# Kernel tuning notes

Hardware: AMD Instinct MI355X
Metric: run time of the kernel (lower is better)

## Reference

```python
import jax, jax.numpy as jnp
import numpy as np

B, S, H = 2, 2048, 3072
NH, NKV, HD = 32, 8, 96
ROPE_THETA = 10000.0
NEG = -1e9


def setup_inputs() -> dict:
    key = jax.random.key(0)
    k0, k1, k2 = jax.random.split(key, 3)
    hidden_states = jax.random.normal(k0, (B, S, H), jnp.float32) * 0.02
    # rotary embeddings (precomputed, as HF passes position_embeddings=(cos,sin))
    inv_freq = 1.0 / (ROPE_THETA ** (jnp.arange(0, HD, 2, dtype=jnp.float32) / HD))
    pos = jnp.arange(S, dtype=jnp.float32)
    freqs = pos[:, None] * inv_freq[None, :]            # [S, HD/2]
    emb = jnp.concatenate([freqs, freqs], axis=-1)      # [S, HD]
    cos = jnp.broadcast_to(jnp.cos(emb)[None], (B, S, HD))
    sin = jnp.broadcast_to(jnp.sin(emb)[None], (B, S, HD))
    # additive causal mask [B,1,S,S]
    causal = jnp.tril(jnp.ones((S, S), dtype=bool))
    attention_mask = jnp.where(causal, 0.0, NEG).astype(jnp.float32)
    attention_mask = jnp.broadcast_to(attention_mask[None, None], (B, 1, S, S))
    Wqkv = jax.random.normal(k1, ((NH + 2 * NKV) * HD, H), jnp.float32) * 0.02
    Wo = jax.random.normal(k2, (H, NH * HD), jnp.float32) * 0.02
    cache_position = jnp.arange(S, dtype=jnp.int32)
    position_ids = jnp.broadcast_to(jnp.arange(S, dtype=jnp.int32)[None], (B, S))
    return {"hidden_states": hidden_states, "cos": cos, "sin": sin,
            "attention_mask": attention_mask, "Wqkv": Wqkv, "Wo": Wo,
            "cache_position": cache_position, "position_ids": position_ids}


def _rotate_half(x):
    x1, x2 = x[..., : HD // 2], x[..., HD // 2:]
    return jnp.concatenate([-x2, x1], axis=-1)


def reference(hidden_states, cos, sin, attention_mask, Wqkv, Wo, cache_position, position_ids):
    # fused qkv projection (no bias in Phi3)
    qkv = jnp.einsum('bsh,dh->bsd', hidden_states, Wqkv)  # [B,S,(NH+2*NKV)*HD]
    q = qkv[..., : NH * HD].reshape(B, S, NH, HD).transpose(0, 2, 1, 3)           # [B,NH,S,HD]
    k = qkv[..., NH * HD: (NH + NKV) * HD].reshape(B, S, NKV, HD).transpose(0, 2, 1, 3)
    v = qkv[..., (NH + NKV) * HD:].reshape(B, S, NKV, HD).transpose(0, 2, 1, 3)   # [B,NKV,S,HD]
    # rotary embedding (unsqueeze head dim)
    cosb, sinb = cos[:, None], sin[:, None]              # [B,1,S,HD]
    q = q * cosb + _rotate_half(q) * sinb
    k = k * cosb + _rotate_half(k) * sinb
    # DynamicCache() is empty -> cache update is identity (k, v unchanged)
    # GQA: repeat kv heads
    rep = NH // NKV
    k = jnp.repeat(k, rep, axis=1)                       # [B,NH,S,HD]
    v = jnp.repeat(v, rep, axis=1)
    # SDPA
    scale = 1.0 / jnp.sqrt(jnp.float32(HD))
    scores = jnp.einsum('bhqd,bhkd->bhqk', q, k) * scale + attention_mask
    attn = jax.nn.softmax(scores, axis=-1)
    ctx = jnp.einsum('bhqk,bhkd->bhqd', attn, v)         # [B,NH,S,HD]
    ctx = ctx.transpose(0, 2, 1, 3).reshape(B, S, NH * HD)
    out = jnp.einsum('bsd,hd->bsh', ctx, Wo)             # o_proj
    return out
```

## Files before the change

### kernel.cpp

```cpp
#include <hip/hip_runtime.h>

typedef __attribute__((ext_vector_type(8))) __bf16 bf16x8;
typedef __attribute__((ext_vector_type(4))) float f32x4;
typedef __attribute__((ext_vector_type(4))) unsigned int u32x4;
typedef __attribute__((ext_vector_type(4))) unsigned short u16x4;
typedef __attribute__((ext_vector_type(8))) unsigned short u16x8;

__device__ __forceinline__ unsigned short f2bf(float x) {
  unsigned u = __builtin_bit_cast(unsigned, x);
  u += 0x7fffu + ((u >> 16) & 1u);
  return (unsigned short)(u >> 16);
}
__device__ __forceinline__ float bf2f(unsigned short h) {
  unsigned u = ((unsigned)h) << 16;
  return __builtin_bit_cast(float, u);
}
__device__ __forceinline__ bf16x8 ld_frag(const unsigned short* p) {
  u32x4 u = *(const u32x4*)p;
  return __builtin_bit_cast(bf16x8, u);
}
__device__ __forceinline__ void gload_lds16(const unsigned short* g, unsigned short* l) {
  __builtin_amdgcn_global_load_lds(
      (const __attribute__((address_space(1))) void*)g,
      (__attribute__((address_space(3))) void*)l, 16, 0, 0);
}

__global__ __launch_bounds__(256) void cvt_bf16(const float* __restrict__ in,
                                                unsigned short* __restrict__ out, int n4) {
  int i = blockIdx.x * 256 + threadIdx.x;
  if (i >= n4) return;
  f32x4 v = *((const f32x4*)in + i);
  u16x4 o;
  #pragma unroll
  for (int j = 0; j < 4; ++j) o[j] = f2bf(v[j]);
  *((u16x4*)out + i) = o;
}

template <int MODE>
__global__ __launch_bounds__(512, 2) void gemm8p(const unsigned short* __restrict__ A,
                                                 const unsigned short* __restrict__ B,
                                                 void* __restrict__ Cv,
                                                 const float* __restrict__ cs,
                                                 const float* __restrict__ sn,
                                                 int M, int N, int K) {
  __shared__ __align__(16) unsigned short SM[57344];
  const int nwg = gridDim.x;
  const int swz = (blockIdx.x & 7) * (nwg >> 3) + (blockIdx.x >> 3);
  const int bx = swz & 15, by = swz >> 4;
  const int row0 = bx * 256, col0 = by * 192;
  const int tid = threadIdx.x;
  const int wave = tid >> 6, lane = tid & 63;
  const int g = lane >> 4, r = lane & 15;
  const int wm = (wave >> 1) * 64, wn = (wave & 1) * 96;
  const int NT = K >> 6;

  const unsigned short* Agb = A + (size_t)row0 * K;
  const unsigned short* Bgb = B + (size_t)col0 * K;

  f32x4 acc[4][6] = {};

  auto SU = [&](const unsigned short* src, unsigned short* dst, int u) {
    const int pos = u * 512 + tid;
    const int rw = pos >> 3, cc = pos & 7;
    gload_lds16(src + (size_t)rw * K + ((cc ^ (rw & 7)) * 8), dst + pos * 8);
  };
  auto LDA = [&](const unsigned short* base, int mi, int dk) {
    const int rw = wm + mi * 16 + r;
    return ld_frag(base + rw * 64 + (((dk * 4 + g) ^ (r & 7)) * 8));
  };
  auto LDB = [&](const unsigned short* base, int ni, int dk) {
    const int rw = wn + ni * 16 + r;
    return ld_frag(base + rw * 64 + (((dk * 4 + g) ^ (r & 7)) * 8));
  };

  SU(Agb, SM, 0); SU(Agb, SM, 1); SU(Agb, SM, 2); SU(Agb, SM, 3);
  SU(Bgb, SM + 16384, 0); SU(Bgb, SM + 16384, 1); SU(Bgb, SM + 16384, 2);
  __syncthreads();

  for (int t = 0; t < NT; ++t) {
    const int d = t & 1;
    const unsigned short* Ab = SM + d * 28672;
    const unsigned short* Bb = Ab + 16384;
    unsigned short* An = SM + (d ^ 1) * 28672;
    unsigned short* Bn = An + 16384;
    const unsigned short* Asrc = Agb + (t + 1) * 64;
    const unsigned short* Bsrc = Bgb + (t + 1) * 64;
    const bool pf = (t + 1 < NT);

    bf16x8 a0, a1, b[6];

    b[0] = LDB(Bb, 0, 0); b[1] = LDB(Bb, 1, 0); b[2] = LDB(Bb, 2, 0);
    b[3] = LDB(Bb, 3, 0); b[4] = LDB(Bb, 4, 0); b[5] = LDB(Bb, 5, 0);
    a0 = LDA(Ab, 0, 0); a1 = LDA(Ab, 1, 0);
    if (pf) { SU(Asrc, An, 0); SU(Asrc, An, 1); SU(Asrc, An, 2); }
    __builtin_amdgcn_s_barrier();
    asm volatile("s_waitcnt lgkmcnt(0)" ::: "memory");
    __builtin_amdgcn_sched_barrier(0);
    __builtin_amdgcn_s_setprio(1);
    #pragma unroll
    for (int n = 0; n < 6; ++n) {
      acc[0][n] = __builtin_amdgcn_mfma_f32_16x16x32_bf16(a0, b[n], acc[0][n], 0, 0, 0);
      acc[1][n] = __builtin_amdgcn_mfma_f32_16x16x32_bf16(a1, b[n], acc[1][n], 0, 0, 0);
    }
    __builtin_amdgcn_s_setprio(0);
    __builtin_amdgcn_s_barrier();

    a0 = LDA(Ab, 2, 0); a1 = LDA(Ab, 3, 0);
    if (pf) { SU(Asrc, An, 3); SU(Bsrc, Bn, 0); }
    __builtin_amdgcn_s_barrier();
    asm volatile("s_waitcnt lgkmcnt(0)" ::: "memory");
    __builtin_amdgcn_sched_barrier(0);
    __builtin_amdgcn_s_setprio(1);
    #pragma unroll
    for (int n = 0; n < 6; ++n) {
      acc[2][n] = __builtin_amdgcn_mfma_f32_16x16x32_bf16(a0, b[n], acc[2][n], 0, 0, 0);
      acc[3][n] = __builtin_amdgcn_mfma_f32_16x16x32_bf16(a1, b[n], acc[3][n], 0, 0, 0);
    }
    __builtin_amdgcn_s_setprio(0);
    __builtin_amdgcn_s_barrier();

    b[0] = LDB(Bb, 0, 1); b[1] = LDB(Bb, 1, 1); b[2] = LDB(Bb, 2, 1);
    b[3] = LDB(Bb, 3, 1); b[4] = LDB(Bb, 4, 1); b[5] = LDB(Bb, 5, 1);
    a0 = LDA(Ab, 0, 1); a1 = LDA(Ab, 1, 1);
    if (pf) { SU(Bsrc, Bn, 1); SU(Bsrc, Bn, 2); }
    __builtin_amdgcn_s_barrier();
    asm volatile("s_waitcnt lgkmcnt(0)" ::: "memory");
    __builtin_amdgcn_sched_barrier(0);
    __builtin_amdgcn_s_setprio(1);
    #pragma unroll
    for (int n = 0; n < 6; ++n) {
      acc[0][n] = __builtin_amdgcn_mfma_f32_16x16x32_bf16(a0, b[n], acc[0][n], 0, 0, 0);
      acc[1][n] = __builtin_amdgcn_mfma_f32_16x16x32_bf16(a1, b[n], acc[1][n], 0, 0, 0);
    }
    __builtin_amdgcn_s_setprio(0);
    __builtin_amdgcn_s_barrier();

    a0 = LDA(Ab, 2, 1); a1 = LDA(Ab, 3, 1);
    __builtin_amdgcn_s_barrier();
    asm volatile("s_waitcnt lgkmcnt(0)" ::: "memory");
    __builtin_amdgcn_sched_barrier(0);
    __builtin_amdgcn_s_setprio(1);
    #pragma unroll
    for (int n = 0; n < 6; ++n) {
      acc[2][n] = __builtin_amdgcn_mfma_f32_16x16x32_bf16(a0, b[n], acc[2][n], 0, 0, 0);
      acc[3][n] = __builtin_amdgcn_mfma_f32_16x16x32_bf16(a1, b[n], acc[3][n], 0, 0, 0);
    }
    __builtin_amdgcn_s_setprio(0);
    asm volatile("s_waitcnt vmcnt(0)" ::: "memory");
    __builtin_amdgcn_s_barrier();
  }

  if (MODE == 0) {
    float* outp = (float*)Cv;
    #pragma unroll
    for (int mi = 0; mi < 4; ++mi)
      #pragma unroll
      for (int n = 0; n < 6; ++n)
        #pragma unroll
        for (int rr = 0; rr < 4; ++rr) {
          const size_t idx = (size_t)(row0 + wm + mi * 16 + g * 4 + rr) * (size_t)N
                           + (col0 + wn + n * 16 + r);
          outp[idx] = acc[mi][n][rr];
        }
  } else {
    unsigned short* outp = (unsigned short*)Cv;
    const int hc0 = col0 + wn;
    if (hc0 < 3840) {
      #pragma unroll
      for (int mi = 0; mi < 4; ++mi)
        #pragma unroll
        for (int rr = 0; rr < 4; ++rr) {
          const int row = row0 + wm + mi * 16 + g * 4 + rr;
          const int cb = row * 96;
          const size_t rb = (size_t)row * N + hc0;
          #pragma unroll
          for (int n = 0; n < 3; ++n) {
            const int d = n * 16 + r;
            const float x1 = acc[mi][n][rr], x2 = acc[mi][n + 3][rr];
            const float c1 = cs[cb + d], s1 = sn[cb + d];
            const float c2 = cs[cb + d + 48], s2 = sn[cb + d + 48];
            outp[rb + d]      = f2bf(x1 * c1 - x2 * s1);
            outp[rb + d + 48] = f2bf(x2 * c2 + x1 * s2);
          }
        }
    } else {
      #pragma unroll
      for (int mi = 0; mi < 4; ++mi)
        #pragma unroll
        for (int n = 0; n < 6; ++n)
          #pragma unroll
          for (int rr = 0; rr < 4; ++rr) {
            const size_t idx = (size_t)(row0 + wm + mi * 16 + g * 4 + rr) * (size_t)N
                             + (col0 + wn + n * 16 + r);
            outp[idx] = f2bf(acc[mi][n][rr]);
          }
    }
  }
}

__global__ __launch_bounds__(256) void vtrans(const unsigned short* __restrict__ qkv,
                                              unsigned short* __restrict__ vt) {
  __shared__ __align__(16) unsigned short T[64 * 104];
  const int s0 = blockIdx.x * 64;
  const int kvh = blockIdx.y, b = blockIdx.z;
  const int tid = threadIdx.x;
  #pragma unroll
  for (int it = 0; it < 3; ++it) {
    const int c = it * 256 + tid;
    const int sr = c / 12, d0 = (c % 12) * 8;
    *(u32x4*)&T[sr * 104 + d0] =
        *(const u32x4*)&qkv[(size_t)(b * 2048 + s0 + sr) * 4608 + 3840 + kvh * 96 + d0];
  }
  __syncthreads();
  #pragma unroll
  for (int it = 0; it < 3; ++it) {
    const int c = it * 256 + tid;
    const int dr = c >> 3, k0 = (c & 7) * 8;
    u16x8 o;
    #pragma unroll
    for (int j = 0; j < 8; ++j) o[j] = T[(k0 + j) * 104 + dr];
    *(u16x8*)&vt[((size_t)(b * 8 + kvh) * 96 + dr) * 2048 + s0 + k0] = o;
  }
}

__global__ __launch_bounds__(512) void attn_fwd(const unsigned short* __restrict__ qkv,
                                                const unsigned short* __restrict__ vt,
                                                unsigned short* __restrict__ ctx) {
  __shared__ __align__(16) unsigned short SMEM[40960];
  const int wg = blockIdx.x;
  const int xcd = wg & 7, j = wg >> 3;
  const int c = xcd + ((j >> 4) << 3);
  const int b = c >> 3, kvh = c & 7;
  const int rj = j & 15;
  const int h = kvh * 4 + (rj >> 2);
  const int pr = rj & 3;
  const int tid = threadIdx.x;
  const int wave = tid >> 6, lane = tid & 63;
  const int g = lane >> 4, r = lane & 15;
  const float kLS = 0.14724445f;

  const unsigned short* kgbase = qkv + (size_t)(b * 2048) * 4608 + 3072 + kvh * 96;
  const unsigned short* vgbase = vt + (size_t)(b * 8 + kvh) * 96 * 2048;

  auto STAGE = [&](int t, int bi) {
    const int kv0 = t * 64;
    unsigned short* kd = SMEM + bi * 6144;
    unsigned short* vd = SMEM + 12288 + bi * 6144;
    #pragma unroll
    for (int i = 0; i < 3; ++i) {
      const int l = i * 512 + tid;
      if (l < 768) {
        const int dk = l >> 8, rem = l & 255;
        const int row = rem >> 2, cc = rem & 3;
        const int csrc = cc ^ ((row >> 1) & 3);
        gload_lds16(kgbase + (size_t)(kv0 + row) * 4608 + dk * 32 + csrc * 8, kd + l * 8);
      } else {
        const int lv = l - 768;
        const int row = lv >> 3, cc = lv & 7;
        const int csrc = cc ^ (row & 7);
        gload_lds16(vgbase + (size_t)row * 2048 + kv0 + csrc * 8, vd + lv * 8);
      }
    }
  };

  #pragma unroll 1
  for (int sel = 0; sel < 2; ++sel) {
    const int qt = sel ? pr : 7 - pr;
    const int nt = qt * 4 + 4;
    const int q0 = qt * 256 + wave * 32;

    __syncthreads();

    bf16x8 qf[2][3];
    #pragma unroll
    for (int qb = 0; qb < 2; ++qb)
      #pragma unroll
      for (int dk = 0; dk < 3; ++dk)
        qf[qb][dk] = ld_frag(&qkv[(size_t)(b * 2048 + q0 + qb * 16 + r) * 4608 + h * 96 + dk * 32 + g * 8]);

    f32x4 o[6][2] = {};
    float m_[2] = {-1e30f, -1e30f};
    float l_[2] = {0.f, 0.f};

    STAGE(0, 0);
    __syncthreads();

    for (int t = 0; t < nt; ++t) {
      const int cur = t & 1;
      if (t + 1 < nt) STAGE(t + 1, cur ^ 1);
      const int kv0 = t * 64;
      const unsigned short* Ks = SMEM + cur * 6144;
      const unsigned short* Vs = SMEM + 12288 + cur * 6144;
      unsigned short* Ps = SMEM + 24576 + wave * 2048;

      if (kv0 <= q0 + 31) {
        f32x4 st[4][2] = {};
        #pragma unroll
        for (int dk = 0; dk < 3; ++dk) {
          bf16x8 af[4];
          #pragma unroll
          for (int kb = 0; kb < 4; ++kb)
            af[kb] = ld_frag(&Ks[dk * 2048 + (kb * 16 + r) * 32 + ((g ^ ((r >> 1) & 3)) * 8)]);
          __builtin_amdgcn_s_setprio(1);
          #pragma unroll
          for (int kb = 0; kb < 4; ++kb)
            #pragma unroll
            for (int qb = 0; qb < 2; ++qb)
              st[kb][qb] = __builtin_amdgcn_mfma_f32_16x16x32_bf16(af[kb], qf[qb][dk], st[kb][qb], 0, 0, 0);
          __builtin_amdgcn_s_setprio(0);
        }
        if (kv0 + 63 > q0) {
          #pragma unroll
          for (int kb = 0; kb < 4; ++kb)
            #pragma unroll
            for (int qb = 0; qb < 2; ++qb)
              #pragma unroll
              for (int rr = 0; rr < 4; ++rr) {
                const int ka = kv0 + kb * 16 + g * 4 + rr;
                const int qa = q0 + qb * 16 + r;
                const float s = st[kb][qb][rr] * kLS;
                st[kb][qb][rr] = (ka <= qa) ? s : -1e30f;
              }
        } else {
          #pragma unroll
          for (int kb = 0; kb < 4; ++kb)
            #pragma unroll
            for (int qb = 0; qb < 2; ++qb)
              #pragma unroll
              for (int rr = 0; rr < 4; ++rr)
                st[kb][qb][rr] *= kLS;
        }
        #pragma unroll
        for (int qb = 0; qb < 2; ++qb) {
          float mx = st[0][qb][0];
          #pragma unroll
          for (int kb = 0; kb < 4; ++kb)
            #pragma unroll
            for (int rr = 0; rr < 4; ++rr) mx = fmaxf(mx, st[kb][qb][rr]);
          mx = fmaxf(mx, __shfl_xor(mx, 16));
          mx = fmaxf(mx, __shfl_xor(mx, 32));
          if (__all(mx <= m_[qb])) {
            float rs = 0.f;
            #pragma unroll
            for (int kb = 0; kb < 4; ++kb)
              #pragma unroll
              for (int rr = 0; rr < 4; ++rr) {
                const float p = __builtin_amdgcn_exp2f(st[kb][qb][rr] - m_[qb]);
                st[kb][qb][rr] = p;
                rs += p;
              }
            rs += __shfl_xor(rs, 16);
            rs += __shfl_xor(rs, 32);
            l_[qb] += rs;
          } else {
            const float mnew = fmaxf(m_[qb], mx);
            const float corr = __builtin_amdgcn_exp2f(m_[qb] - mnew);
            m_[qb] = mnew;
            float rs = 0.f;
            #pragma unroll
            for (int kb = 0; kb < 4; ++kb)
              #pragma unroll
              for (int rr = 0; rr < 4; ++rr) {
                const float p = __builtin_amdgcn_exp2f(st[kb][qb][rr] - mnew);
                st[kb][qb][rr] = p;
                rs += p;
              }
            rs += __shfl_xor(rs, 16);
            rs += __shfl_xor(rs, 32);
            l_[qb] = l_[qb] * corr + rs;
            #pragma unroll
            for (int db = 0; db < 6; ++db) o[db][qb] *= corr;
          }
        }
        #pragma unroll
        for (int kb = 0; kb < 4; ++kb)
          #pragma unroll
          for (int qb = 0; qb < 2; ++qb) {
            u16x4 w;
            #pragma unroll
            for (int rr = 0; rr < 4; ++rr) w[rr] = f2bf(st[kb][qb][rr]);
            const int q = qb * 16 + r;
            *(u16x4*)&Ps[q * 64 + (((2 * kb + (g >> 1)) ^ (r & 7)) << 3) + (g & 1) * 4] = w;
          }
        #pragma unroll
        for (int kk = 0; kk < 2; ++kk) {
          bf16x8 pb[2];
          #pragma unroll
          for (int qb = 0; qb < 2; ++qb)
            pb[qb] = ld_frag(&Ps[(qb * 16 + r) * 64 + ((kk * 4 + g) ^ (r & 7)) * 8]);
          __builtin_amdgcn_s_setprio(1);
          #pragma unroll
          for (int db = 0; db < 6; ++db) {
            const bf16x8 va = ld_frag(&Vs[(db * 16 + r) * 64 + ((kk * 4 + g) ^ (r & 7)) * 8]);
            #pragma unroll
            for (int qb = 0; qb < 2; ++qb)
              o[db][qb] = __builtin_amdgcn_mfma_f32_16x16x32_bf16(va, pb[qb], o[db][qb], 0, 0, 0);
          }
          __builtin_amdgcn_s_setprio(0);
        }
      }
      __syncthreads();
    }

    const float inv_l[2] = {1.f / l_[0], 1.f / l_[1]};
    unsigned short* obuf = SMEM + wave * 3328;
    #pragma unroll
    for (int db = 0; db < 6; ++db)
      #pragma unroll
      for (int qb = 0; qb < 2; ++qb) {
        u16x4 w;
        #pragma unroll
        for (int rr = 0; rr < 4; ++rr) w[rr] = f2bf(o[db][qb][rr] * inv_l[qb]);
        *(u16x4*)&obuf[(qb * 16 + r) * 104 + db * 16 + g * 4] = w;
      }
    #pragma unroll
    for (int it = 0; it < 6; ++it) {
      const int cc = it * 64 + lane;
      const int qr = cc / 12, d0 = (cc % 12) * 8;
      *(u32x4*)&ctx[(size_t)(b * 2048 + q0 + qr) * 3072 + h * 96 + d0] =
          *(const u32x4*)&obuf[qr * 104 + d0];
    }
  }
}

extern "C" void kernel_launch(void* const* d_in, const int* in_sizes, int n_in,
                              void* d_out, int out_size, void* d_ws, size_t ws_size,
                              hipStream_t stream) {
  const float* hs   = (const float*)d_in[0];
  const float* cosp = (const float*)d_in[1];
  const float* sinp = (const float*)d_in[2];
  const float* wqkv = (const float*)d_in[4];
  const float* wo   = (const float*)d_in[5];
  float* out = (float*)d_out;

  unsigned short* qkv = (unsigned short*)d_ws;
  unsigned short* hsb = qkv + 18874368;
  unsigned short* wqb = hsb + 12582912;
  unsigned short* vt  = hsb;
  unsigned short* wob = hsb + 3145728;
  unsigned short* ctx = wqb;

  cvt_bf16<<<12288, 256, 0, stream>>>(hs,   hsb, 3145728);
  cvt_bf16<<<13824, 256, 0, stream>>>(wqkv, wqb, 3538944);
  gemm8p<1><<<384, 512, 0, stream>>>(hsb, wqb, (void*)qkv, cosp, sinp, 4096, 4608, 3072);
  vtrans<<<dim3(32, 8, 2), 256, 0, stream>>>(qkv, vt);
  cvt_bf16<<<9216, 256, 0, stream>>>(wo, wob, 2359296);
  attn_fwd<<<256, 512, 0, stream>>>(qkv, vt, ctx);
  gemm8p<0><<<256, 512, 0, stream>>>(ctx, wob, (void*)out, cosp, sinp, 4096, 3072, 3072);
}
```

Baseline: 342.3 us.

## Add 4-wave 128x192-tile GEMM for QKV projection with RoPE epilogue

Adds a new gemm4w kernel using 256-thread blocks with a 128x192 output tile and a double-buffered LDS pipeline, and uses it for the fused QKV projection plus RoPE instead of the 8-wave gemm8p. The grid doubles to 768 smaller workgroups, which improves wave-quantization and load balance across CUs and may allow more blocks per CU. In exchange each block reuses less data, so global/LDS traffic per FLOP rises.

Result: slower. 402.6 us (+17.6%).

```diff
diff --git a/kernel.cpp b/kernel.cpp
--- a/kernel.cpp
+++ b/kernel.cpp
@@ -123,6 +123,169 @@
     b[3] = LDB(Bb, 3, 1); b[4] = LDB(Bb, 4, 1); b[5] = LDB(Bb, 5, 1);
     a0 = LDA(Ab, 0, 1); a1 = LDA(Ab, 1, 1);
     if (pf) { SU(Bsrc, Bn, 1); SU(Bsrc, Bn, 2); }
+    __builtin_amdgcn_s_barrier();
+    asm volatile("s_waitcnt lgkmcnt(0)" ::: "memory");
+    __builtin_amdgcn_sched_barrier(0);
+    __builtin_amdgcn_s_setprio(1);
+    #pragma unroll
+    for (int n = 0; n < 6; ++n) {
+      acc[0][n] = __builtin_amdgcn_mfma_f32_16x16x32_bf16(a0, b[n], acc[0][n], 0, 0, 0);
+      acc[1][n] = __builtin_amdgcn_mfma_f32_16x16x32_bf16(a1, b[n], acc[1][n], 0, 0, 0);
+    }
+    __builtin_amdgcn_s_setprio(0);
+    __builtin_amdgcn_s_barrier();
+
+    a0 = LDA(Ab, 2, 1); a1 = LDA(Ab, 3, 1);
+    __builtin_amdgcn_s_barrier();
+    asm volatile("s_waitcnt lgkmcnt(0)" ::: "memory");
+    __builtin_amdgcn_sched_barrier(0);
+    __builtin_amdgcn_s_setprio(1);
+    #pragma unroll
+    for (int n = 0; n < 6; ++n) {
+      acc[2][n] = __builtin_amdgcn_mfma_f32_16x16x32_bf16(a0, b[n], acc[2][n], 0, 0, 0);
+      acc[3][n] = __builtin_amdgcn_mfma_f32_16x16x32_bf16(a1, b[n], acc[3][n], 0, 0, 0);
+    }
+    __builtin_amdgcn_s_setprio(0);
+    asm volatile("s_waitcnt vmcnt(0)" ::: "memory");
+    __builtin_amdgcn_s_barrier();
+  }
+
+  if (MODE == 0) {
+    float* outp = (float*)Cv;
+    #pragma unroll
+    for (int mi = 0; mi < 4; ++mi)
+      #pragma unroll
+      for (int n = 0; n < 6; ++n)
+        #pragma unroll
+        for (int rr = 0; rr < 4; ++rr) {
+          const size_t idx = (size_t)(row0 + wm + mi * 16 + g * 4 + rr) * (size_t)N
+                           + (col0 + wn + n * 16 + r);
+          outp[idx] = acc[mi][n][rr];
+        }
+  } else {
+    unsigned short* outp = (unsigned short*)Cv;
+    const int hc0 = col0 + wn;
+    if (hc0 < 3840) {
+      #pragma unroll
+      for (int mi = 0; mi < 4; ++mi)
+        #pragma unroll
+        for (int rr = 0; rr < 4; ++rr) {
+          const int row = row0 + wm + mi * 16 + g * 4 + rr;
+          const int cb = row * 96;
+          const size_t rb = (size_t)row * N + hc0;
+          #pragma unroll
+          for (int n = 0; n < 3; ++n) {
+            const int d = n * 16 + r;
+            const float x1 = acc[mi][n][rr], x2 = acc[mi][n + 3][rr];
+            const float c1 = cs[cb + d], s1 = sn[cb + d];
+            const float c2 = cs[cb + d + 48], s2 = sn[cb + d + 48];
+            outp[rb + d]      = f2bf(x1 * c1 - x2 * s1);
+            outp[rb + d + 48] = f2bf(x2 * c2 + x1 * s2);
+          }
+        }
+    } else {
+      #pragma unroll
+      for (int mi = 0; mi < 4; ++mi)
+        #pragma unroll
+        for (int n = 0; n < 6; ++n)
+          #pragma unroll
+          for (int rr = 0; rr < 4; ++rr) {
+            const size_t idx = (size_t)(row0 + wm + mi * 16 + g * 4 + rr) * (size_t)N
+                             + (col0 + wn + n * 16 + r);
+            outp[idx] = f2bf(acc[mi][n][rr]);
+          }
+    }
+  }
+}
+
+template <int MODE>
+__global__ __launch_bounds__(256) void gemm4w(const unsigned short* __restrict__ A,
+                                              const unsigned short* __restrict__ B,
+                                              void* __restrict__ Cv,
+                                              const float* __restrict__ cs,
+                                              const float* __restrict__ sn,
+                                              int M, int N, int K) {
+  __shared__ __align__(16) unsigned short SM[40960];
+  const int nwg = gridDim.x;
+  const int swz = (blockIdx.x & 7) * (nwg >> 3) + (blockIdx.x >> 3);
+  const int bx = swz & 31, by = swz >> 5;
+  const int row0 = bx * 128, col0 = by * 192;
+  const int tid = threadIdx.x;
+  const int wave = tid >> 6, lane = tid & 63;
+  const int g = lane >> 4, r = lane & 15;
+  const int wm = (wave >> 1) * 64, wn = (wave & 1) * 96;
+  const int NT = K >> 6;
+
+  const unsigned short* Agb = A + (size_t)row0 * K;
+  const unsigned short* Bgb = B + (size_t)col0 * K;
+
+  f32x4 acc[4][6] = {};
+
+  auto SU = [&](const unsigned short* src, unsigned short* dst, int u) {
+    const int pos = u * 256 + tid;
+    const int rw = pos >> 3, cc = pos & 7;
+    gload_lds16(src + (size_t)rw * K + ((cc ^ (rw & 7)) * 8), dst + pos * 8);
+  };
+  auto LDA = [&](const unsigned short* base, int mi, int dk) {
+    const int rw = wm + mi * 16 + r;
+    return ld_frag(base + rw * 64 + (((dk * 4 + g) ^ (r & 7)) * 8));
+  };
+  auto LDB = [&](const unsigned short* base, int ni, int dk) {
+    const int rw = wn + ni * 16 + r;
+    return ld_frag(base + rw * 64 + (((dk * 4 + g) ^ (r & 7)) * 8));
+  };
+
+  SU(Agb, SM, 0); SU(Agb, SM, 1); SU(Agb, SM, 2); SU(Agb, SM, 3);
+  SU(Bgb, SM + 8192, 0); SU(Bgb, SM + 8192, 1); SU(Bgb, SM + 8192, 2);
+  SU(Bgb, SM + 8192, 3); SU(Bgb, SM + 8192, 4); SU(Bgb, SM + 8192, 5);
+  __syncthreads();
+
+  for (int t = 0; t < NT; ++t) {
+    const int d = t & 1;
+    const unsigned short* Ab = SM + d * 20480;
+    const unsigned short* Bb = Ab + 8192;
+    unsigned short* An = SM + (d ^ 1) * 20480;
+    unsigned short* Bn = An + 8192;
+    const unsigned short* Asrc = Agb + (t + 1) * 64;
+    const unsigned short* Bsrc = Bgb + (t + 1) * 64;
+    const bool pf = (t + 1 < NT);
+
+    bf16x8 a0, a1, b[6];
+
+    b[0] = LDB(Bb, 0, 0); b[1] = LDB(Bb, 1, 0); b[2] = LDB(Bb, 2, 0);
+    b[3] = LDB(Bb, 3, 0); b[4] = LDB(Bb, 4, 0); b[5] = LDB(Bb, 5, 0);
+    a0 = LDA(Ab, 0, 0); a1 = LDA(Ab, 1, 0);
+    if (pf) { SU(Asrc, An, 0); SU(Asrc, An, 1); SU(Asrc, An, 2); SU(Asrc, An, 3); }
+    __builtin_amdgcn_s_barrier();
+    asm volatile("s_waitcnt lgkmcnt(0)" ::: "memory");
+    __builtin_amdgcn_sched_barrier(0);
+    __builtin_amdgcn_s_setprio(1);
+    #pragma unroll
+    for (int n = 0; n < 6; ++n) {
+      acc[0][n] = __builtin_amdgcn_mfma_f32_16x16x32_bf16(a0, b[n], acc[0][n], 0, 0, 0);
+      acc[1][n] = __builtin_amdgcn_mfma_f32_16x16x32_bf16(a1, b[n], acc[1][n], 0, 0, 0);
+    }
+    __builtin_amdgcn_s_setprio(0);
+    __builtin_amdgcn_s_barrier();
+
+    a0 = LDA(Ab, 2, 0); a1 = LDA(Ab, 3, 0);
+    if (pf) { SU(Bsrc, Bn, 0); SU(Bsrc, Bn, 1); SU(Bsrc, Bn, 2); }
+    __builtin_amdgcn_s_barrier();
+    asm volatile("s_waitcnt lgkmcnt(0)" ::: "memory");
+    __builtin_amdgcn_sched_barrier(0);
+    __builtin_amdgcn_s_setprio(1);
+    #pragma unroll
+    for (int n = 0; n < 6; ++n) {
+      acc[2][n] = __builtin_amdgcn_mfma_f32_16x16x32_bf16(a0, b[n], acc[2][n], 0, 0, 0);
+      acc[3][n] = __builtin_amdgcn_mfma_f32_16x16x32_bf16(a1, b[n], acc[3][n], 0, 0, 0);
+    }
+    __builtin_amdgcn_s_setprio(0);
+    __builtin_amdgcn_s_barrier();
+
+    b[0] = LDB(Bb, 0, 1); b[1] = LDB(Bb, 1, 1); b[2] = LDB(Bb, 2, 1);
+    b[3] = LDB(Bb, 3, 1); b[4] = LDB(Bb, 4, 1); b[5] = LDB(Bb, 5, 1);
+    a0 = LDA(Ab, 0, 1); a1 = LDA(Ab, 1, 1);
+    if (pf) { SU(Bsrc, Bn, 3); SU(Bsrc, Bn, 4); SU(Bsrc, Bn, 5); }
     __builtin_amdgcn_s_barrier();
     asm volatile("s_waitcnt lgkmcnt(0)" ::: "memory");
     __builtin_amdgcn_sched_barrier(0);
@@ -442,7 +605,7 @@
 
   cvt_bf16<<<12288, 256, 0, stream>>>(hs,   hsb, 3145728);
   cvt_bf16<<<13824, 256, 0, stream>>>(wqkv, wqb, 3538944);
-  gemm8p<1><<<384, 512, 0, stream>>>(hsb, wqb, (void*)qkv, cosp, sinp, 4096, 4608, 3072);
+  gemm4w<1><<<768, 256, 0, stream>>>(hsb, wqb, (void*)qkv, cosp, sinp, 4096, 4608, 3072);
   vtrans<<<dim3(32, 8, 2), 256, 0, stream>>>(qkv, vt);
   cvt_bf16<<<9216, 256, 0, stream>>>(wo, wob, 2359296);
   attn_fwd<<<256, 512, 0, stream>>>(qkv, vt, ctx);
```

## Fuse input conversions and overlap Wo conversion with QKV GEMM

Applied to the files above, without the earlier changes.

Merges the hidden-state and Wqkv fp32-to-bf16 conversions into one launch. When the workspace is large enough, it appends extra blocks to the QKV GEMM grid that convert Wo concurrently with the GEMM, which removes a separate launch and overlaps that memory-bound work. It also shifts the prefetch issue schedule so all A and B tile loads are issued in the first two sub-phases. The extra conversion blocks compete with GEMM blocks for CUs, and the earlier prefetch raises in-flight load pressure.

Measured after the change: 346.0 us. Within noise of the previous version (+1.1%).

```diff
diff --git a/kernel.cpp b/kernel.cpp
--- a/kernel.cpp
+++ b/kernel.cpp
@@ -36,15 +36,53 @@
   *((u16x4*)out + i) = o;
 }
 
+__global__ __launch_bounds__(256) void cvt2_bf16(const float* __restrict__ a,
+                                                 unsigned short* __restrict__ oa, int na4,
+                                                 const float* __restrict__ b,
+                                                 unsigned short* __restrict__ ob, int nb4) {
+  const int i = blockIdx.x * 256 + threadIdx.x;
+  if (i < na4) {
+    f32x4 v = *((const f32x4*)a + i);
+    u16x4 o;
+    #pragma unroll
+    for (int j = 0; j < 4; ++j) o[j] = f2bf(v[j]);
+    *((u16x4*)oa + i) = o;
+  } else {
+    const int k = i - na4;
+    if (k < nb4) {
+      f32x4 v = *((const f32x4*)b + k);
+      u16x4 o;
+      #pragma unroll
+      for (int j = 0; j < 4; ++j) o[j] = f2bf(v[j]);
+      *((u16x4*)ob + k) = o;
+    }
+  }
+}
+
 template <int MODE>
 __global__ __launch_bounds__(512, 2) void gemm8p(const unsigned short* __restrict__ A,
                                                  const unsigned short* __restrict__ B,
                                                  void* __restrict__ Cv,
                                                  const float* __restrict__ cs,
                                                  const float* __restrict__ sn,
-                                                 int M, int N, int K) {
+                                                 int M, int N, int K,
+                                                 const float* __restrict__ cvt_src,
+                                                 unsigned short* __restrict__ cvt_dst,
+                                                 int cvt_n4, int gemm_blocks) {
   __shared__ __align__(16) unsigned short SM[57344];
-  const int nwg = gridDim.x;
+  if ((int)blockIdx.x >= gemm_blocks) {
+    const int nthr = ((int)gridDim.x - gemm_blocks) * 512;
+    for (int i = ((int)blockIdx.x - gemm_blocks) * 512 + (int)threadIdx.x;
+         i < cvt_n4; i += nthr) {
+      f32x4 v = *((const f32x4*)cvt_src + i);
+      u16x4 o;
+      #pragma unroll
+      for (int j = 0; j < 4; ++j) o[j] = f2bf(v[j]);
+      *((u16x4*)cvt_dst + i) = o;
+    }
+    return;
+  }
+  const int nwg = gemm_blocks;
   const int swz = (blockIdx.x & 7) * (nwg >> 3) + (blockIdx.x >> 3);
   const int bx = swz & 15, by = swz >> 4;
   const int row0 = bx * 256, col0 = by * 192;
@@ -92,7 +130,7 @@
     b[0] = LDB(Bb, 0, 0); b[1] = LDB(Bb, 1, 0); b[2] = LDB(Bb, 2, 0);
     b[3] = LDB(Bb, 3, 0); b[4] = LDB(Bb, 4, 0); b[5] = LDB(Bb, 5, 0);
     a0 = LDA(Ab, 0, 0); a1 = LDA(Ab, 1, 0);
-    if (pf) { SU(Asrc, An, 0); SU(Asrc, An, 1); SU(Asrc, An, 2); }
+    if (pf) { SU(Asrc, An, 0); SU(Asrc, An, 1); SU(Asrc, An, 2); SU(Asrc, An, 3); }
     __builtin_amdgcn_s_barrier();
     asm volatile("s_waitcnt lgkmcnt(0)" ::: "memory");
     __builtin_amdgcn_sched_barrier(0);
@@ -106,7 +144,7 @@
     __builtin_amdgcn_s_barrier();
 
     a0 = LDA(Ab, 2, 0); a1 = LDA(Ab, 3, 0);
-    if (pf) { SU(Asrc, An, 3); SU(Bsrc, Bn, 0); }
+    if (pf) { SU(Bsrc, Bn, 0); SU(Bsrc, Bn, 1); SU(Bsrc, Bn, 2); }
     __builtin_amdgcn_s_barrier();
     asm volatile("s_waitcnt lgkmcnt(0)" ::: "memory");
     __builtin_amdgcn_sched_barrier(0);
@@ -122,7 +160,6 @@
     b[0] = LDB(Bb, 0, 1); b[1] = LDB(Bb, 1, 1); b[2] = LDB(Bb, 2, 1);
     b[3] = LDB(Bb, 3, 1); b[4] = LDB(Bb, 4, 1); b[5] = LDB(Bb, 5, 1);
     a0 = LDA(Ab, 0, 1); a1 = LDA(Ab, 1, 1);
-    if (pf) { SU(Bsrc, Bn, 1); SU(Bsrc, Bn, 2); }
     __builtin_amdgcn_s_barrier();
     asm volatile("s_waitcnt lgkmcnt(0)" ::: "memory");
     __builtin_amdgcn_sched_barrier(0);
@@ -437,14 +474,22 @@
   unsigned short* hsb = qkv + 18874368;
   unsigned short* wqb = hsb + 12582912;
   unsigned short* vt  = hsb;
-  unsigned short* wob = hsb + 3145728;
   unsigned short* ctx = wqb;
 
-  cvt_bf16<<<12288, 256, 0, stream>>>(hs,   hsb, 3145728);
-  cvt_bf16<<<13824, 256, 0, stream>>>(wqkv, wqb, 3538944);
-  gemm8p<1><<<384, 512, 0, stream>>>(hsb, wqb, (void*)qkv, cosp, sinp, 4096, 4608, 3072);
+  const bool big_ws = ws_size >= (size_t)110100480;
+  unsigned short* wob = big_ws ? (wqb + 14155776) : (hsb + 3145728);
+
+  cvt2_bf16<<<26112, 256, 0, stream>>>(hs, hsb, 3145728, wqkv, wqb, 3538944);
+  if (big_ws) {
+    gemm8p<1><<<512, 512, 0, stream>>>(hsb, wqb, (void*)qkv, cosp, sinp, 4096, 4608, 3072,
+                                       wo, wob, 2359296, 384);
+  } else {
+    gemm8p<1><<<384, 512, 0, stream>>>(hsb, wqb, (void*)qkv, cosp, sinp, 4096, 4608, 3072,
+                                       nullptr, nullptr, 0, 384);
+    cvt_bf16<<<9216, 256, 0, stream>>>(wo, wob, 2359296);
+  }
   vtrans<<<dim3(32, 8, 2), 256, 0, stream>>>(qkv, vt);
-  cvt_bf16<<<9216, 256, 0, stream>>>(wo, wob, 2359296);
   attn_fwd<<<256, 512, 0, stream>>>(qkv, vt, ctx);
-  gemm8p<0><<<256, 512, 0, stream>>>(ctx, wob, (void*)out, cosp, sinp, 4096, 3072, 3072);
-}
+  gemm8p<0><<<256, 512, 0, stream>>>(ctx, wob, (void*)out, cosp, sinp, 4096, 3072, 3072,
+                                     nullptr, nullptr, 0, 256);
+}
```
